# Optimization experiments

Measured on AMD Instinct MI355X. Metric: run time of the kernel, lower is better.

Reference implementation:

```python
import jax, jax.numpy as jnp
import numpy as np

EMBED = 512
LATENT = 32
N_HEADS = 16  # 16 identical SelfAttention layers, concatenated
VOCAB = 32000
LN_EPS = 1e-5


def setup_inputs() -> dict:
    key = jax.random.key(0)
    ks = jax.random.split(key, 12)
    B, S = 2, 2048
    f32 = jnp.float32
    n = lambda k, sh, s=1.0: (jax.random.normal(k, sh, dtype=f32) * s)
    return {
        "Q": n(ks[0], (B, S, EMBED)),
        "K": n(ks[1], (B, S, EMBED)),
        "V": n(ks[2], (B, S, EMBED)),
        "X": n(ks[3], (B, S, EMBED)),
        # latent_downscale: Linear(512 -> 32)
        "Wd": n(ks[4], (EMBED, LATENT), 0.02), "bd": jnp.zeros((LATENT,), f32),
        # latent_upscale: Linear(32 -> 512)
        "Wu": n(ks[5], (LATENT, EMBED), 0.02), "bu": jnp.zeros((EMBED,), f32),
        # LayerNorm(512)
        "gamma": jnp.ones((EMBED,), f32), "beta": jnp.zeros((EMBED,), f32),
        # final_linear_layer: Linear(512 -> vocab)
        "Wf": n(ks[6], (EMBED, VOCAB), 0.02), "bf": jnp.zeros((VOCAB,), f32),
    }


def reference(Q, K, V, X, Wd, bd, Wu, bu, gamma, beta, Wf, bf):
    # Downscale all streams to latent dim 32
    q = Q @ Wd + bd  # [B,S,L]
    k = K @ Wd + bd
    v = V @ Wd + bd
    x = X @ Wd + bd

    B, S, L = q.shape
    # Causal attention, scale by sqrt(latent dim) as in the original (dim = 32)
    scores = jnp.einsum("bqd,bkd->bqk", q, k) / jnp.sqrt(jnp.asarray(L, q.dtype))
    causal = jnp.triu(jnp.ones((S, S), dtype=bool), k=1)  # True above diagonal
    scores = jnp.where(causal, -jnp.inf, scores)
    weights = jax.nn.softmax(scores, axis=-1)
    ctx = jnp.einsum("bqk,bkd->bqd", weights, v)  # [B,S,L]

    # All 16 attention layers receive identical (q,k,v): concat == tile x16
    combined = jnp.tile(ctx, (1, 1, N_HEADS))  # [B,S,512]

    enc = combined + (x @ Wu + bu)
    # LayerNorm over last dim
    mu = jnp.mean(enc, axis=-1, keepdims=True)
    var = jnp.mean((enc - mu) ** 2, axis=-1, keepdims=True)
    enc = (enc - mu) * jax.lax.rsqrt(var + LN_EPS) * gamma + beta

    return enc @ Wf + bf  # [B,S,VOCAB]
```

## Files before the change

### kernel.cpp

```cpp
#include <hip/hip_runtime.h>

#define EMBED 512
#define LATENT 32
#define SEQ 2048
#define MTOT 4096
#define VOCAB 32000

typedef float f32x4 __attribute__((ext_vector_type(4)));
typedef short s16x8 __attribute__((ext_vector_type(8)));

__device__ __forceinline__ unsigned short f2bf(float f) {
  unsigned u = __float_as_uint(f);
  u += 0x7FFFu + ((u >> 16) & 1u);
  return (unsigned short)(u >> 16);
}

__device__ __forceinline__ void mfma16x16x32(f32x4& d, s16x8 a, s16x8 b) {
  asm("v_mfma_f32_16x16x32_bf16 %0, %1, %2, %0" : "+v"(d) : "v"(a), "v"(b));
}

__device__ __forceinline__ void gload16(const void* g, void* l) {
  __builtin_amdgcn_global_load_lds(
      (const __attribute__((address_space(1))) void*)g,
      (__attribute__((address_space(3))) void*)l, 16, 0, 0);
}

__global__ __launch_bounds__(256) void k_downscale(
    const float* __restrict__ Q, const float* __restrict__ K,
    const float* __restrict__ V, const float* __restrict__ X,
    const float* __restrict__ Wd, const float* __restrict__ bd,
    float* __restrict__ latq, float* __restrict__ latk,
    float* __restrict__ latv, float* __restrict__ latx) {
  __shared__ float wdT[32][516];
  const float* in; float* out;
  switch (blockIdx.y) {
    case 0: in = Q; out = latq; break;
    case 1: in = K; out = latk; break;
    case 2: in = V; out = latv; break;
    default: in = X; out = latx; break;
  }
  int t = threadIdx.x;
#pragma unroll
  for (int j = 0; j < 16; ++j) {
    int q = t * 64 + j * 4;
    f32x4 v = *(const f32x4*)(Wd + q);
    int k = q >> 5, c = q & 31;
    wdT[c + 0][k] = v.x;
    wdT[c + 1][k] = v.y;
    wdT[c + 2][k] = v.z;
    wdT[c + 3][k] = v.w;
  }
  __syncthreads();
  int r = t >> 5, c = t & 31;
  int row = blockIdx.x * 8 + r;
  const float* rowp = in + (size_t)row * EMBED;
  float acc = 0.f;
#pragma unroll 8
  for (int k = 0; k < 512; k += 4) {
    f32x4 iv = *(const f32x4*)(rowp + k);
    f32x4 wv = *(const f32x4*)&wdT[c][k];
    acc += iv.x * wv.x + iv.y * wv.y + iv.z * wv.z + iv.w * wv.w;
  }
  out[(size_t)row * 32 + c] = acc + bd[c];
}

__global__ __launch_bounds__(256) void k_attn(
    const float* __restrict__ lq, const float* __restrict__ lk,
    const float* __restrict__ lv, float* __restrict__ ctx) {
  __shared__ char kvbuf[4][16384];
  int lane = threadIdx.x & 63;
  int lw = threadIdx.x >> 6;
  int bl = blockIdx.x;
  int qg;
  switch (lw) {
    case 0: qg = bl; break;
    case 1: qg = 2047 - bl; break;
    case 2: qg = 2048 + bl; break;
    default: qg = 4095 - bl; break;
  }
  int batch = qg >> 11;
  int qi = qg & 2047;
  const float* qp = lq + (size_t)qg * 32;
  f32x4 q4[8], ca[8];
#pragma unroll
  for (int d = 0; d < 8; ++d) {
    q4[d] = *(const f32x4*)(qp + d * 4);
    ca[d] = f32x4{0.f, 0.f, 0.f, 0.f};
  }
  const char* kbp = (const char*)(lk + (size_t)batch * SEQ * 32);
  const char* vbp = (const char*)(lv + (size_t)batch * SEQ * 32);
  char* kl = kvbuf[lw];
  char* vl = kvbuf[lw] + 8192;

  auto stage = [&](int j0) {
#pragma unroll
    for (int i = 0; i < 8; ++i) {
      int o = i * 1024 + lane * 16;
      int row = o >> 7;
      int sb = (((o >> 4) & 7) ^ (row & 7)) << 4;
      gload16(kbp + (size_t)(j0 + row) * 128 + sb, kl + o);
    }
#pragma unroll
    for (int i = 0; i < 8; ++i) {
      int o = i * 1024 + lane * 16;
      int row = o >> 7;
      int sb = (((o >> 4) & 7) ^ (row & 7)) << 4;
      gload16(vbp + (size_t)(j0 + row) * 128 + sb, vl + o);
    }
  };

  float m = -INFINITY, ssum = 0.f;
  const float scale = 0.17677669529663687f;
  int nChunk = (qi >> 6) + 1;

  stage(0);
  asm volatile("s_waitcnt vmcnt(0)" ::: "memory");

  for (int c = 0; c < nChunk; ++c) {
    f32x4 kr[8], vr[8];
#pragma unroll
    for (int d = 0; d < 8; ++d) {
      int sb = (d ^ (lane & 7)) << 4;
      kr[d] = *(const f32x4*)(kl + lane * 128 + sb);
      vr[d] = *(const f32x4*)(vl + lane * 128 + sb);
    }
    asm volatile("s_waitcnt lgkmcnt(0)" ::: "memory");
    __builtin_amdgcn_sched_barrier(0);
    if (c + 1 < nChunk) stage((c + 1) * 64);
    __builtin_amdgcn_sched_barrier(0);
    int j = c * 64 + lane;
    if (j <= qi) {
      f32x4 s4 = f32x4{0.f, 0.f, 0.f, 0.f};
#pragma unroll
      for (int d = 0; d < 8; ++d) s4 += q4[d] * kr[d];
      float s = (s4.x + s4.y + s4.z + s4.w) * scale;
      float mn = fmaxf(m, s);
      float f = __expf(m - mn);
      float p = __expf(s - mn);
      ssum = ssum * f + p;
#pragma unroll
      for (int d = 0; d < 8; ++d) ca[d] = ca[d] * f + p * vr[d];
      m = mn;
    }
    if (c + 1 < nChunk)
      asm volatile("s_waitcnt vmcnt(0)" ::: "memory");
  }

  float M = m;
#pragma unroll
  for (int off = 32; off > 0; off >>= 1) M = fmaxf(M, __shfl_xor(M, off, 64));
  float sc = (m == -INFINITY) ? 0.f : __expf(m - M);
  ssum *= sc;
#pragma unroll
  for (int off = 32; off > 0; off >>= 1) ssum += __shfl_xor(ssum, off, 64);
#pragma unroll
  for (int d = 0; d < 8; ++d) {
    ca[d] *= sc;
#pragma unroll
    for (int off = 32; off > 0; off >>= 1) {
      ca[d].x += __shfl_xor(ca[d].x, off, 64);
      ca[d].y += __shfl_xor(ca[d].y, off, 64);
      ca[d].z += __shfl_xor(ca[d].z, off, 64);
      ca[d].w += __shfl_xor(ca[d].w, off, 64);
    }
  }
  float inv = 1.f / ssum;
  float outv = 0.f;
#pragma unroll
  for (int d = 0; d < 32; ++d) {
    if (lane == d) outv = ca[d >> 2][d & 3];
  }
  if (lane < 32) ctx[(size_t)qg * 32 + lane] = outv * inv;
}

__global__ __launch_bounds__(512) void k_upln(
    const float* __restrict__ ctx, const float* __restrict__ latx,
    const float* __restrict__ Wu, const float* __restrict__ bu,
    const float* __restrict__ gamma, const float* __restrict__ beta,
    unsigned short* __restrict__ encb) {
  int r = blockIdx.x;
  int c = threadIdx.x;
  float acc = bu[c] + ctx[(size_t)r * 32 + (c & 31)];
  const float* lx = latx + (size_t)r * 32;
#pragma unroll
  for (int k = 0; k < 32; ++k) acc += lx[k] * Wu[k * EMBED + c];
  int lane = threadIdx.x & 63, w = threadIdx.x >> 6;
  float s1 = acc, s2 = acc * acc;
#pragma unroll
  for (int off = 32; off > 0; off >>= 1) {
    s1 += __shfl_xor(s1, off, 64);
    s2 += __shfl_xor(s2, off, 64);
  }
  __shared__ float r1[8], r2[8];
  if (lane == 0) { r1[w] = s1; r2[w] = s2; }
  __syncthreads();
  float t1 = 0.f, t2 = 0.f;
#pragma unroll
  for (int i = 0; i < 8; ++i) { t1 += r1[i]; t2 += r2[i]; }
  float mu = t1 * (1.f / 512.f);
  float var = t2 * (1.f / 512.f) - mu * mu;
  float rstd = rsqrtf(var + 1e-5f);
  float o = (acc - mu) * rstd * gamma[c] + beta[c];
  encb[(size_t)r * EMBED + c] = f2bf(o);
}

__global__ __launch_bounds__(256) void k_transcast(
    const float* __restrict__ Wf, unsigned short* __restrict__ wfT) {
  __shared__ float tile[64][65];
  int n0 = blockIdx.x * 64;
  int k0 = blockIdx.y * 64;
  int t = threadIdx.x;
  int rr = t >> 4;
  int cq = (t & 15) << 2;
#pragma unroll
  for (int p = 0; p < 4; ++p) {
    int kr = p * 16 + rr;
    f32x4 v = *(const f32x4*)(Wf + (size_t)(k0 + kr) * VOCAB + n0 + cq);
    tile[kr][cq + 0] = v.x;
    tile[kr][cq + 1] = v.y;
    tile[kr][cq + 2] = v.z;
    tile[kr][cq + 3] = v.w;
  }
  __syncthreads();
#pragma unroll
  for (int p = 0; p < 4; ++p) {
    int nr = p * 16 + rr;
    ushort4 u;
    u.x = f2bf(tile[cq + 0][nr]);
    u.y = f2bf(tile[cq + 1][nr]);
    u.z = f2bf(tile[cq + 2][nr]);
    u.w = f2bf(tile[cq + 3][nr]);
    *(ushort4*)(wfT + (size_t)(n0 + nr) * EMBED + k0 + cq) = u;
  }
}

__global__ __launch_bounds__(512, 4) void k_gemm(
    const unsigned short* __restrict__ A,
    const unsigned short* __restrict__ Bt,
    const float* __restrict__ bias, float* __restrict__ C) {
  __shared__ char lds[2][24576];
  int tid = threadIdx.x;
  int lane = tid & 63, wave = tid >> 6;
  int wm = wave & 3, wn = wave >> 2;
  int fr = lane & 15, fq = lane >> 4;
  int kswz = (fq ^ ((fr >> 1) & 3)) << 4;

  int id = blockIdx.x;
  int nid = (id & 7) * 500 + (id >> 3);
  int bm = nid & 15, bn = nid >> 4;
  int m0 = bm * 256, n0 = bn * 128;

  const char* Ab = (const char*)(A + (size_t)m0 * EMBED);
  const char* Bb = (const char*)(Bt + (size_t)n0 * EMBED);

  f32x4 acc[4][4];
#pragma unroll
  for (int i = 0; i < 4; ++i)
#pragma unroll
    for (int j = 0; j < 4; ++j) acc[i][j] = f32x4{0.f, 0.f, 0.f, 0.f};

  auto stage = [&](char* slot, int koff) {
#pragma unroll
    for (int i = 0; i < 2; ++i) {
      int o = i * 8192 + tid * 16;
      int row = o >> 6;
      int kb = (((o >> 4) & 3) ^ ((row >> 1) & 3)) << 4;
      gload16(Ab + (size_t)row * 1024 + koff + kb, slot + o);
    }
    int o = tid * 16;
    int row = o >> 6;
    int kb = (((o >> 4) & 3) ^ ((row >> 1) & 3)) << 4;
    gload16(Bb + (size_t)row * 1024 + koff + kb, slot + 16384 + o);
  };

  stage(&lds[0][0], 0);
  asm volatile("s_waitcnt vmcnt(0)" ::: "memory");
  __builtin_amdgcn_s_barrier();

  for (int kt = 0; kt < 16; ++kt) {
    const char* Ar = &lds[kt & 1][0];
    const char* Br = Ar + 16384;
    if (kt < 15) stage(&lds[(kt + 1) & 1][0], (kt + 1) * 64);
    s16x8 af[4];
#pragma unroll
    for (int mi = 0; mi < 4; ++mi) {
      int row = wm * 64 + mi * 16 + fr;
      af[mi] = *(const s16x8*)(Ar + row * 64 + kswz);
    }
    __builtin_amdgcn_s_setprio(1);
#pragma unroll
    for (int ni = 0; ni < 4; ++ni) {
      int row = wn * 64 + ni * 16 + fr;
      s16x8 bf = *(const s16x8*)(Br + row * 64 + kswz);
#pragma unroll
      for (int mi = 0; mi < 4; ++mi) mfma16x16x32(acc[mi][ni], af[mi], bf);
    }
    __builtin_amdgcn_s_setprio(0);
    asm volatile("s_waitcnt vmcnt(0)" ::: "memory");
    __builtin_amdgcn_s_barrier();
  }

  float* ep = (float*)&lds[0][0] + wave * 1088;
  float bvv[4];
#pragma unroll
  for (int ni = 0; ni < 4; ++ni) bvv[ni] = bias[n0 + wn * 64 + ni * 16 + fr];
#pragma unroll
  for (int mi = 0; mi < 4; ++mi) {
#pragma unroll
    for (int ni = 0; ni < 4; ++ni)
#pragma unroll
      for (int r = 0; r < 4; ++r)
        ep[(fq * 4 + r) * 68 + ni * 16 + fr] = acc[mi][ni][r] + bvv[ni];
    __builtin_amdgcn_sched_barrier(0);
    asm volatile("s_waitcnt lgkmcnt(0)" ::: "memory");
    __builtin_amdgcn_sched_barrier(0);
#pragma unroll
    for (int p = 0; p < 4; ++p) {
      int row = p * 4 + fq;
      f32x4 v = *(const f32x4*)(ep + row * 68 + fr * 4);
      int m = m0 + wm * 64 + mi * 16 + row;
      __builtin_nontemporal_store(
          v, (f32x4*)(C + (size_t)m * VOCAB + n0 + wn * 64 + fr * 4));
    }
    __builtin_amdgcn_sched_barrier(0);
    asm volatile("s_waitcnt lgkmcnt(0)" ::: "memory");
    __builtin_amdgcn_sched_barrier(0);
  }
}

extern "C" void kernel_launch(void* const* d_in, const int* in_sizes, int n_in,
                              void* d_out, int out_size, void* d_ws,
                              size_t ws_size, hipStream_t stream) {
  (void)in_sizes; (void)n_in; (void)out_size; (void)ws_size;
  const float* Q = (const float*)d_in[0];
  const float* K = (const float*)d_in[1];
  const float* V = (const float*)d_in[2];
  const float* X = (const float*)d_in[3];
  const float* Wd = (const float*)d_in[4];
  const float* bd = (const float*)d_in[5];
  const float* Wu = (const float*)d_in[6];
  const float* bu = (const float*)d_in[7];
  const float* gamma = (const float*)d_in[8];
  const float* beta = (const float*)d_in[9];
  const float* Wf = (const float*)d_in[10];
  const float* bf = (const float*)d_in[11];
  float* out = (float*)d_out;
  char* ws = (char*)d_ws;
  float* latq = (float*)(ws + 0);
  float* latk = (float*)(ws + (1u << 19));
  float* latv = (float*)(ws + (2u << 19));
  float* latx = (float*)(ws + 3u * (1u << 19));
  float* ctx = (float*)(ws + (1u << 21));
  unsigned short* encb = (unsigned short*)(ws + (1u << 21) + (1u << 19));
  unsigned short* wfT =
      (unsigned short*)(ws + (1u << 21) + (1u << 19) + (1u << 22));

  k_downscale<<<dim3(512, 4), 256, 0, stream>>>(Q, K, V, X, Wd, bd, latq,
                                                latk, latv, latx);
  k_transcast<<<dim3(VOCAB / 64, EMBED / 64), 256, 0, stream>>>(Wf, wfT);
  k_attn<<<1024, 256, 0, stream>>>(latq, latk, latv, ctx);
  k_upln<<<MTOT, 512, 0, stream>>>(ctx, latx, Wu, bu, gamma, beta, encb);
  k_gemm<<<4000, 512, 0, stream>>>(encb, wfT, bf, out);
}
```

Baseline: 302.8 us.

## Load GEMM A fragments directly to registers and amortize downscale weight transpose

The vocab GEMM no longer stages the A (activation) tile through LDS. Each wave now loads its A fragments straight from global memory into registers, double-buffered one k-step ahead, and only B goes through a smaller double-buffered LDS region with partial vmcnt waits. This cuts LDS traffic and LDS footprint per block, but adds redundant global reads of A across the two wn waves and more register pressure. Separately, the downscale kernel processes four row groups per block with a quarter of the blocks, amortizing the per-block Wd transpose into shared memory.

Result: slower. 402.1 us (+32.8%).

```diff
diff --git a/kernel.cpp b/kernel.cpp
--- a/kernel.cpp
+++ b/kernel.cpp
@@ -52,16 +52,19 @@
   }
   __syncthreads();
   int r = t >> 5, c = t & 31;
-  int row = blockIdx.x * 8 + r;
-  const float* rowp = in + (size_t)row * EMBED;
-  float acc = 0.f;
+#pragma unroll 1
+  for (int p = 0; p < 4; ++p) {
+    int row = blockIdx.x * 32 + p * 8 + r;
+    const float* rowp = in + (size_t)row * EMBED;
+    float acc = 0.f;
 #pragma unroll 8
-  for (int k = 0; k < 512; k += 4) {
-    f32x4 iv = *(const f32x4*)(rowp + k);
-    f32x4 wv = *(const f32x4*)&wdT[c][k];
-    acc += iv.x * wv.x + iv.y * wv.y + iv.z * wv.z + iv.w * wv.w;
-  }
-  out[(size_t)row * 32 + c] = acc + bd[c];
+    for (int k = 0; k < 512; k += 4) {
+      f32x4 iv = *(const f32x4*)(rowp + k);
+      f32x4 wv = *(const f32x4*)&wdT[c][k];
+      acc += iv.x * wv.x + iv.y * wv.y + iv.z * wv.z + iv.w * wv.w;
+    }
+    out[(size_t)row * 32 + c] = acc + bd[c];
+  }
 }
 
 __global__ __launch_bounds__(256) void k_attn(
@@ -238,7 +241,7 @@
     const unsigned short* __restrict__ A,
     const unsigned short* __restrict__ Bt,
     const float* __restrict__ bias, float* __restrict__ C) {
-  __shared__ char lds[2][24576];
+  __shared__ char lds[34816];
   int tid = threadIdx.x;
   int lane = tid & 63, wave = tid >> 6;
   int wm = wave & 3, wn = wave >> 2;
@@ -259,48 +262,82 @@
 #pragma unroll
     for (int j = 0; j < 4; ++j) acc[i][j] = f32x4{0.f, 0.f, 0.f, 0.f};
 
-  auto stage = [&](char* slot, int koff) {
-#pragma unroll
-    for (int i = 0; i < 2; ++i) {
-      int o = i * 8192 + tid * 16;
-      int row = o >> 6;
-      int kb = (((o >> 4) & 3) ^ ((row >> 1) & 3)) << 4;
-      gload16(Ab + (size_t)row * 1024 + koff + kb, slot + o);
-    }
+  auto stageB = [&](char* slot, int koff) {
     int o = tid * 16;
     int row = o >> 6;
     int kb = (((o >> 4) & 3) ^ ((row >> 1) & 3)) << 4;
-    gload16(Bb + (size_t)row * 1024 + koff + kb, slot + 16384 + o);
+    gload16(Bb + (size_t)row * 1024 + koff + kb, slot + o);
   };
-
-  stage(&lds[0][0], 0);
+  auto loadA = [&](s16x8* af, int kt) {
+#pragma unroll
+    for (int mi = 0; mi < 4; ++mi) {
+      int row = wm * 64 + mi * 16 + fr;
+      af[mi] = *(const s16x8*)(Ab + (size_t)row * 1024 + kt * 64 + fq * 16);
+    }
+  };
+  auto dsB = [&](s16x8* bfr, const char* slot) {
+#pragma unroll
+    for (int ni = 0; ni < 4; ++ni) {
+      int row = wn * 64 + ni * 16 + fr;
+      bfr[ni] = *(const s16x8*)(slot + row * 64 + kswz);
+    }
+  };
+
+  char* slot0 = &lds[0];
+  char* slot1 = &lds[8192];
+  s16x8 af0[4], af1[4], bfr[4];
+
+  stageB(slot0, 0);
+  loadA(af0, 0);
   asm volatile("s_waitcnt vmcnt(0)" ::: "memory");
   __builtin_amdgcn_s_barrier();
 
-  for (int kt = 0; kt < 16; ++kt) {
-    const char* Ar = &lds[kt & 1][0];
-    const char* Br = Ar + 16384;
-    if (kt < 15) stage(&lds[(kt + 1) & 1][0], (kt + 1) * 64);
-    s16x8 af[4];
-#pragma unroll
-    for (int mi = 0; mi < 4; ++mi) {
-      int row = wm * 64 + mi * 16 + fr;
-      af[mi] = *(const s16x8*)(Ar + row * 64 + kswz);
-    }
-    __builtin_amdgcn_s_setprio(1);
-#pragma unroll
-    for (int ni = 0; ni < 4; ++ni) {
-      int row = wn * 64 + ni * 16 + fr;
-      s16x8 bf = *(const s16x8*)(Br + row * 64 + kswz);
-#pragma unroll
-      for (int mi = 0; mi < 4; ++mi) mfma16x16x32(acc[mi][ni], af[mi], bf);
-    }
-    __builtin_amdgcn_s_setprio(0);
-    asm volatile("s_waitcnt vmcnt(0)" ::: "memory");
-    __builtin_amdgcn_s_barrier();
-  }
-
-  float* ep = (float*)&lds[0][0] + wave * 1088;
+#pragma unroll 1
+  for (int t2 = 0; t2 < 8; ++t2) {
+    int kt = t2 * 2;
+    {
+      if (kt < 15) {
+        stageB(slot1, (kt + 1) * 64);
+        loadA(af1, kt + 1);
+      }
+      dsB(bfr, slot0);
+      __builtin_amdgcn_s_setprio(1);
+#pragma unroll
+      for (int ni = 0; ni < 4; ++ni)
+#pragma unroll
+        for (int mi = 0; mi < 4; ++mi)
+          mfma16x16x32(acc[mi][ni], af0[mi], bfr[ni]);
+      __builtin_amdgcn_s_setprio(0);
+      __builtin_amdgcn_sched_barrier(0);
+      if (kt < 15) {
+        asm volatile("s_waitcnt vmcnt(4)" ::: "memory");
+        __builtin_amdgcn_s_barrier();
+      }
+    }
+    {
+      int ko = kt + 1;
+      if (ko < 15) {
+        stageB(slot0, (ko + 1) * 64);
+        loadA(af0, ko + 1);
+      }
+      dsB(bfr, slot1);
+      __builtin_amdgcn_s_setprio(1);
+#pragma unroll
+      for (int ni = 0; ni < 4; ++ni)
+#pragma unroll
+        for (int mi = 0; mi < 4; ++mi)
+          mfma16x16x32(acc[mi][ni], af1[mi], bfr[ni]);
+      __builtin_amdgcn_s_setprio(0);
+      __builtin_amdgcn_sched_barrier(0);
+      if (ko < 15) {
+        asm volatile("s_waitcnt vmcnt(4)" ::: "memory");
+        __builtin_amdgcn_s_barrier();
+      }
+    }
+  }
+  __builtin_amdgcn_s_barrier();
+
+  float* ep = (float*)&lds[0] + wave * 1088;
   float bvv[4];
 #pragma unroll
   for (int ni = 0; ni < 4; ++ni) bvv[ni] = bias[n0 + wn * 64 + ni * 16 + fr];
@@ -355,7 +392,7 @@
   unsigned short* wfT =
       (unsigned short*)(ws + (1u << 21) + (1u << 19) + (1u << 22));
 
-  k_downscale<<<dim3(512, 4), 256, 0, stream>>>(Q, K, V, X, Wd, bd, latq,
+  k_downscale<<<dim3(128, 4), 256, 0, stream>>>(Q, K, V, X, Wd, bd, latq,
                                                 latk, latv, latx);
   k_transcast<<<dim3(VOCAB / 64, EMBED / 64), 256, 0, stream>>>(Wf, wfT);
   k_attn<<<1024, 256, 0, stream>>>(latq, latk, latv, ctx);
```
